# Kernel tuning notes

Hardware: AMD Instinct MI355X
Metric: run time of the kernel (lower is better)

Reference implementation:

```python
import jax, jax.numpy as jnp
import numpy as np

D_MODEL = 1024
D_INNER = 2048   # expand * d_model
D_STATE = 16
D_CONV = 4
DT_RANK = 64     # ceil(d_model / 16)
BATCH = 4
SEQ = 4096


def setup_inputs() -> dict:
    key = jax.random.key(0)
    ks = jax.random.split(key, 8)
    nrm = lambda k, shape, scale: jax.random.normal(k, shape, jnp.float32) * scale
    # dt_proj bias init (inverse softplus of dt in [dt_min, dt_max])
    dt_min, dt_max, dt_floor = 1e-3, 1e-1, 1e-4
    dt = jnp.exp(jax.random.uniform(ks[5], (D_INNER,), jnp.float32)
                 * (np.log(dt_max) - np.log(dt_min)) + np.log(dt_min))
    dt = jnp.clip(dt, dt_floor, None)
    b_dt = dt + jnp.log(-jnp.expm1(-dt))
    # A = diag(1..d_state) per channel, stored as log
    A_log = jnp.broadcast_to(jnp.log(jnp.arange(1, D_STATE + 1, dtype=jnp.float32))[None, :],
                             (D_INNER, D_STATE)).copy()
    dt_std = DT_RANK ** -0.5
    return {
        "x": nrm(ks[0], (BATCH, SEQ, D_MODEL), 1.0),
        "W_in": nrm(ks[1], (2 * D_INNER, D_MODEL), 0.02),
        "conv_w": nrm(ks[2], (D_INNER, 1, D_CONV), 0.2),
        "conv_b": jnp.zeros((D_INNER,), jnp.float32),
        "W_x": nrm(ks[3], (DT_RANK + 2 * D_STATE, D_INNER), 0.02),
        "W_dt": jax.random.uniform(ks[4], (D_INNER, DT_RANK), jnp.float32, -dt_std, dt_std),
        "b_dt": b_dt,
        "A_log": A_log,
        "D": jnp.ones((D_INNER,), jnp.float32),
        "W_out": nrm(ks[6], (D_MODEL, D_INNER), 0.02),
    }


def reference(x, W_in, conv_w, conv_b, W_x, W_dt, b_dt, A_log, D, W_out):
    B, T, _ = x.shape
    silu = jax.nn.silu
    # in_proj -> (x_inner, z)
    xz = jnp.einsum('btd,ed->bte', x, W_in)          # (B,T,2*d_inner)
    x_inner, z = jnp.split(xz, 2, axis=-1)
    # causal depthwise conv1d (pad left d_conv-1, equiv to torch pad+slice[:T])
    xp = jnp.pad(x_inner.transpose(0, 2, 1), ((0, 0), (0, 0), (D_CONV - 1, 0)))
    xc = jax.lax.conv_general_dilated(xp, conv_w, (1,), 'VALID',
                                      feature_group_count=D_INNER)  # (B,d_inner,T)
    x_conv = silu(xc + conv_b[None, :, None]).transpose(0, 2, 1)    # (B,T,d_inner)
    # x_proj -> dt_rank | B | C
    x_dbl = jnp.einsum('btd,ed->bte', x_conv, W_x)
    dt_r, B_ssm, C_ssm = jnp.split(x_dbl, [DT_RANK, DT_RANK + D_STATE], axis=-1)
    dt = jax.nn.softplus(jnp.einsum('btr,dr->btd', dt_r, W_dt) + b_dt)  # (B,T,d_inner)
    A = -jnp.exp(A_log)                                                 # (d_inner,d_state)
    # selective scan over time
    def step(s, inp):
        x_t, dt_t, B_t, C_t = inp              # (B,d_inner),(B,d_inner),(B,d_state),(B,d_state)
        dA = jnp.exp(dt_t[:, :, None] * A[None])              # (B,d_inner,d_state)
        s = s * dA + (dt_t * x_t)[:, :, None] * B_t[:, None, :]
        y_t = jnp.einsum('bds,bs->bd', s, C_t)
        return s, y_t

    s0 = jnp.zeros((B, D_INNER, D_STATE), jnp.float32)
    scan_in = (x_conv.transpose(1, 0, 2), dt.transpose(1, 0, 2),
               B_ssm.transpose(1, 0, 2), C_ssm.transpose(1, 0, 2))
    _, ys = jax.lax.scan(step, s0, scan_in)    # (T,B,d_inner)
    y = ys.transpose(1, 0, 2)
    y = y * silu(z) + D * x_conv
    out = jnp.einsum('btd,ed->bte', y, W_out)  # (B,T,d_model)
    return out
```

## Files before the change

kernel.cpp:

```cpp
#include <hip/hip_runtime.h>
#include <hip/hip_bf16.h>
#include <hip/hip_fp16.h>

#define SEQ    4096
#define DMODEL 1024
#define DINNER 2048
#define DSTATE 16
#define DTRANK 64
#define NC     64
#define CL     64
#define SPLITK 4

typedef __bf16 v8bf  __attribute__((ext_vector_type(8)));
typedef float  f32x4 __attribute__((ext_vector_type(4)));
typedef unsigned short u16x8 __attribute__((ext_vector_type(8)));

static __device__ __forceinline__ float bfu2f(unsigned short u) {
    union { float f; unsigned int i; } c; c.i = ((unsigned int)u) << 16; return c.f;
}
static __device__ __forceinline__ unsigned short f2bfu(float f) {
    union { float f; unsigned int i; } c; c.f = f;
    unsigned int r = c.i + 0x7FFFu + ((c.i >> 16) & 1u);
    return (unsigned short)(r >> 16);
}
static __device__ __forceinline__ float h2f(unsigned short u) {
    __half h; *reinterpret_cast<unsigned short*>(&h) = u; return __half2float(h);
}
static __device__ __forceinline__ unsigned short f2h(float f) {
    __half h = __float2half(f); return *reinterpret_cast<unsigned short*>(&h);
}
static __device__ __forceinline__ float softplus_fast(float v) {
    return fmaxf(v, 0.f) + __logf(1.f + __expf(-fabsf(v)));
}

static __device__ __forceinline__ void gload_lds16(const void* g, void* l) {
    __builtin_amdgcn_global_load_lds(
        (const __attribute__((address_space(1))) unsigned int*)g,
        (__attribute__((address_space(3))) unsigned int*)l, 16, 0, 0);
}

static __device__ __forceinline__ void pow16(float e1, float* pw) {
    const float e2 = e1 * e1, e4 = e2 * e2, e8 = e4 * e4;
    pw[0] = e1;        pw[1] = e2;        pw[2] = e2 * e1;   pw[3] = e4;
    pw[4] = e4 * e1;   pw[5] = e4 * e2;   pw[6] = e4 * pw[2]; pw[7] = e8;
    pw[8] = e8 * e1;   pw[9] = e8 * e2;   pw[10] = e8 * pw[2]; pw[11] = e8 * e4;
    pw[12] = e8 * pw[4]; pw[13] = e8 * pw[5]; pw[14] = e8 * pw[6]; pw[15] = e8 * e8;
}

__global__ void detect_kernel(const void* __restrict__ x, int* __restrict__ flag)
{
    const float f = ((const float*)x)[threadIdx.x];
    const float a = fabsf(f);
    const bool ok = (a < 1e20f) && (a > 1e-20f);
    unsigned long long m = __ballot(ok);
    if (threadIdx.x == 0) *flag = (__popcll(m) >= 48) ? 1 : 0;
}

__global__ void prep_kernel(const unsigned short* __restrict__ a_log_b,
                            int* __restrict__ sflag)
{
    __shared__ int ok_sh;
    if (threadIdx.x == 0) ok_sh = 1;
    __syncthreads();
    int ok = 1;
    for (int i = threadIdx.x; i < DINNER * DSTATE; i += 256) {
        const float A = __expf(bfu2f(a_log_b[i]));
        const float n = (float)((i & 15) + 1);
        if (fabsf(A - n) > 0.02f * n) ok = 0;
    }
    if (!ok) atomicAnd(&ok_sh, 0);
    __syncthreads();
    if (threadIdx.x == 0) *sflag = ok_sh;
}

__global__ __launch_bounds__(256) void cvt_kernel(
    const void* __restrict__ src, size_t src_off,
    unsigned short* __restrict__ dst, int n, const int* __restrict__ flagp)
{
    const int f32 = *flagp;
    const int stride = gridDim.x * 256;
    if (f32) {
        const float* s = (const float*)src + src_off;
        for (int i = blockIdx.x * 256 + threadIdx.x; i < n; i += stride)
            dst[i] = f2bfu(s[i]);
    } else {
        const unsigned short* s = (const unsigned short*)src + src_off;
        for (int i = blockIdx.x * 256 + threadIdx.x; i < n; i += stride)
            dst[i] = s[i];
    }
}

struct CvtBatch {
    const void* src[9];
    unsigned short* dst[9];
    int n[9];
};
__global__ __launch_bounds__(256) void cvt9_kernel(CvtBatch jb,
                                                   const int* __restrict__ flagp)
{
    const int f32 = *flagp;
    const int t = blockIdx.y;
    const int n = jb.n[t];
    unsigned short* __restrict__ dst = jb.dst[t];
    const int stride = gridDim.x * 256;
    if (f32) {
        const float* __restrict__ s = (const float*)jb.src[t];
        for (int i = blockIdx.x * 256 + threadIdx.x; i < n; i += stride)
            dst[i] = f2bfu(s[i]);
    } else {
        const unsigned short* __restrict__ s = (const unsigned short*)jb.src[t];
        for (int i = blockIdx.x * 256 + threadIdx.x; i < n; i += stride)
            dst[i] = s[i];
    }
}

__global__ __launch_bounds__(256) void gemm_db(
    const unsigned short* __restrict__ A, int lda,
    const unsigned short* __restrict__ B, int ldb,
    void* __restrict__ Cbase, int row0c, int ldc, int c_ext,
    int N, int K, const int* __restrict__ flagp, int nfast)
{
    __shared__ __align__(16) unsigned short SM[4 * 128 * 64];

    const int cf32 = c_ext ? *flagp : 0;

    const int tid  = threadIdx.x;
    const int lane = tid & 63;
    const int wave = tid >> 6;
    const int wr   = wave >> 1;
    const int wc   = wave & 1;

    const int bid = blockIdx.y * gridDim.x + blockIdx.x;
    const int r   = bid & 7;
    const int q   = bid >> 3;
    int mt, nt;
    if (nfast) {
        const int npx = gridDim.x;
        const int qm  = q / npx;
        mt = r * (gridDim.y >> 3) + qm;
        nt = q - qm * npx;
    } else {
        const int mpx = gridDim.y >> 3;
        mt = r * mpx + (q & (mpx - 1));
        nt = q / mpx;
    }
    const int m0  = mt * 128;
    const int n0  = nt * 128;

    f32x4 acc[4][4] = {};

    const int r32 = tid >> 3;
    const int c8  = tid & 7;

    const unsigned short* Arow = A + (size_t)m0 * lda;
    const unsigned short* Brow = B + (size_t)n0 * ldb;

#define STAGE_DB(buf, k0)                                                      \
    {                                                                          \
        _Pragma("unroll")                                                      \
        for (int h = 0; h < 4; ++h) {                                          \
            const int rr = r32 + h * 32;                                       \
            const int lg = (c8 ^ (rr & 7)) * 8;                                \
            gload_lds16(&Arow[(size_t)rr * lda + (k0) + lg],                   \
                        &SM[(buf) * 8192 + rr * 64 + c8 * 8]);                 \
            gload_lds16(&Brow[(size_t)rr * ldb + (k0) + lg],                   \
                        &SM[16384 + (buf) * 8192 + rr * 64 + c8 * 8]);         \
        }                                                                      \
    }

    STAGE_DB(0, 0);
    const int NT = K >> 6;
    int cur = 0;

    for (int kt = 0; kt < NT; ++kt) {
        if (kt + 1 < NT) {
            STAGE_DB(cur ^ 1, (kt + 1) * 64);
            asm volatile("s_waitcnt vmcnt(8)" ::: "memory");
        } else {
            asm volatile("s_waitcnt vmcnt(0)" ::: "memory");
        }
        __builtin_amdgcn_s_barrier();

        const unsigned short* Ab = &SM[cur * 8192];
        const unsigned short* Bb = &SM[16384 + cur * 8192];
        const int lm = lane & 15;
        const int g  = lane >> 4;
#pragma unroll
        for (int ks = 0; ks < 2; ++ks) {
            v8bf a_frag[4], b_frag[4];
#pragma unroll
            for (int i = 0; i < 4; ++i) {
                const int ra = wr * 64 + i * 16 + lm;
                const int rb = wc * 64 + i * 16 + lm;
                a_frag[i] = *reinterpret_cast<const v8bf*>(
                    &Ab[ra * 64 + (((ks * 4 + g) ^ (ra & 7))) * 8]);
                b_frag[i] = *reinterpret_cast<const v8bf*>(
                    &Bb[rb * 64 + (((ks * 4 + g) ^ (rb & 7))) * 8]);
            }
#pragma unroll
            for (int i = 0; i < 4; ++i)
#pragma unroll
                for (int j = 0; j < 4; ++j)
                    acc[i][j] = __builtin_amdgcn_mfma_f32_16x16x32_bf16(
                        a_frag[i], b_frag[j], acc[i][j], 0, 0, 0);
        }
        asm volatile("" ::: "memory");
        __builtin_amdgcn_s_barrier();
        cur ^= 1;
    }
#undef STAGE_DB

    float* eb = reinterpret_cast<float*>(SM);
    {
        const int lm = lane & 15;
        const int lr = (lane >> 4) * 4;
#pragma unroll
        for (int i = 0; i < 4; ++i)
#pragma unroll
            for (int j = 0; j < 4; ++j) {
                const int cl = wc * 64 + j * 16 + lm;
#pragma unroll
                for (int q2 = 0; q2 < 4; ++q2) {
                    const int row = wr * 64 + i * 16 + lr + q2;
                    eb[row * 128 + (cl ^ ((row & 7) << 2))] = acc[i][j][q2];
                }
            }
    }
    __syncthreads();
#pragma unroll
    for (int r0 = 0; r0 < 8; ++r0) {
        const int row = (tid >> 4) + r0 * 16;
        const int cb2 = (tid & 15) * 8;
        const int sw  = (row & 7) << 2;
        const f32x4 v0 = *reinterpret_cast<const f32x4*>(&eb[row * 128 + (cb2 ^ sw)]);
        const f32x4 v1 = *reinterpret_cast<const f32x4*>(&eb[row * 128 + ((cb2 + 4) ^ sw)]);
        const size_t gr = (size_t)(row0c + m0 + row) * ldc + n0 + cb2;
        if (cf32) {
            __builtin_nontemporal_store(v0, reinterpret_cast<f32x4*>(&((float*)Cbase)[gr]));
            __builtin_nontemporal_store(v1, reinterpret_cast<f32x4*>(&((float*)Cbase)[gr + 4]));
        } else {
            u16x8 o;
#pragma unroll
            for (int k = 0; k < 4; ++k) { o[k] = f2bfu(v0[k]); o[4 + k] = f2bfu(v1[k]); }
            *reinterpret_cast<u16x8*>(&((unsigned short*)Cbase)[gr]) = o;
        }
    }
}

__global__ __launch_bounds__(256) void gemm_dt(
    const unsigned short* __restrict__ A, int lda,
    const unsigned short* __restrict__ B, int ldb,
    unsigned short* __restrict__ Cbase, int ldc,
    const unsigned short* __restrict__ bias)
{
    __shared__ __align__(16) unsigned short SM[2 * 128 * 64];

    const int tid  = threadIdx.x;
    const int lane = tid & 63;
    const int wave = tid >> 6;
    const int wr   = wave >> 1;
    const int wc   = wave & 1;
    const int m0   = blockIdx.y * 128;
    const int n0   = blockIdx.x * 128;

    f32x4 acc[4][4] = {};

    const int r32 = tid >> 3;
    const int c8  = tid & 7;

    unsigned short* As = SM;
    unsigned short* Bs = SM + 8192;
    {
#pragma unroll
        for (int h = 0; h < 4; ++h) {
            const int rr = r32 + h * 32;
            const int lg = (c8 ^ (rr & 7)) * 8;
            gload_lds16(&A[(size_t)(m0 + rr) * lda + lg], &As[rr * 64 + c8 * 8]);
            gload_lds16(&B[(size_t)(n0 + rr) * ldb + lg], &Bs[rr * 64 + c8 * 8]);
        }
        __syncthreads();

        const int lm = lane & 15;
        const int g  = lane >> 4;
#pragma unroll
        for (int ks = 0; ks < 2; ++ks) {
            v8bf a_frag[4], b_frag[4];
#pragma unroll
            for (int i = 0; i < 4; ++i) {
                const int ra = wr * 64 + i * 16 + lm;
                const int rb = wc * 64 + i * 16 + lm;
                a_frag[i] = *reinterpret_cast<const v8bf*>(
                    &As[ra * 64 + (((ks * 4 + g) ^ (ra & 7))) * 8]);
                b_frag[i] = *reinterpret_cast<const v8bf*>(
                    &Bs[rb * 64 + (((ks * 4 + g) ^ (rb & 7))) * 8]);
            }
#pragma unroll
            for (int i = 0; i < 4; ++i)
#pragma unroll
                for (int j = 0; j < 4; ++j)
                    acc[i][j] = __builtin_amdgcn_mfma_f32_16x16x32_bf16(
                        a_frag[i], b_frag[j], acc[i][j], 0, 0, 0);
        }
    }

    __syncthreads();
    unsigned short* eb16 = SM;
    {
        const int lm = lane & 15;
        const int lr = (lane >> 4) * 4;
#pragma unroll
        for (int i = 0; i < 4; ++i)
#pragma unroll
            for (int j = 0; j < 4; ++j) {
                const int cl = wc * 64 + j * 16 + lm;
                const float bv = bfu2f(bias[n0 + cl]);
#pragma unroll
                for (int q = 0; q < 4; ++q) {
                    const int row = wr * 64 + i * 16 + lr + q;
                    const int pos = row * 128 +
                        ((((cl >> 3) ^ (row & 7)) << 3) | (cl & 7));
                    eb16[pos] = f2h(softplus_fast(acc[i][j][q] + bv));
                }
            }
    }
    __syncthreads();
#pragma unroll
    for (int r0 = 0; r0 < 8; ++r0) {
        const int row = (tid >> 4) + r0 * 16;
        const int ch  = tid & 15;
        const u16x8 v = *reinterpret_cast<const u16x8*>(
            &eb16[row * 128 + ((ch ^ (row & 7)) << 3)]);
        *reinterpret_cast<u16x8*>(
            &Cbase[(size_t)(m0 + row) * ldc + n0 + ch * 8]) = v;
    }
}

__global__ __launch_bounds__(256) void gemm_splitk(
    const unsigned short* __restrict__ A, int lda,
    const unsigned short* __restrict__ B, int ldb,
    float* __restrict__ part, int Mrows,
    int N, int kchunk)
{
    __shared__ __align__(16) unsigned short SM[4 * 128 * 64];

    const int tid  = threadIdx.x;
    const int lane = tid & 63;
    const int wave = tid >> 6;
    const int wr   = wave >> 1;
    const int wc   = wave & 1;
    const int m0   = blockIdx.y * 128;
    const int split = blockIdx.z;
    const int kbeg = split * kchunk;

    f32x4 acc[4][4] = {};

    const int r32 = tid >> 3;
    const int c8  = tid & 7;

#define STAGE_SK(buf, k0)                                                      \
    {                                                                          \
        _Pragma("unroll")                                                      \
        for (int h = 0; h < 4; ++h) {                                          \
            const int rr = r32 + h * 32;                                       \
            const int lg = (c8 ^ (rr & 7)) * 8;                                \
            gload_lds16(&A[(size_t)(m0 + rr) * lda + (k0) + lg],               \
                        &SM[(buf) * 8192 + rr * 64 + c8 * 8]);                 \
            gload_lds16(&B[(size_t)rr * ldb + (k0) + lg],                      \
                        &SM[16384 + (buf) * 8192 + rr * 64 + c8 * 8]);         \
        }                                                                      \
    }

    STAGE_SK(0, kbeg);
    const int NT = kchunk >> 6;
    int cur = 0;

    for (int kt = 0; kt < NT; ++kt) {
        if (kt + 1 < NT) {
            STAGE_SK(cur ^ 1, kbeg + (kt + 1) * 64);
            asm volatile("s_waitcnt vmcnt(8)" ::: "memory");
        } else {
            asm volatile("s_waitcnt vmcnt(0)" ::: "memory");
        }
        __builtin_amdgcn_s_barrier();

        const unsigned short* Ab = &SM[cur * 8192];
        const unsigned short* Bb = &SM[16384 + cur * 8192];
        const int lm = lane & 15;
        const int g  = lane >> 4;
#pragma unroll
        for (int ks = 0; ks < 2; ++ks) {
            v8bf a_frag[4], b_frag[4];
#pragma unroll
            for (int i = 0; i < 4; ++i) {
                const int ra = wr * 64 + i * 16 + lm;
                const int rb = wc * 64 + i * 16 + lm;
                a_frag[i] = *reinterpret_cast<const v8bf*>(
                    &Ab[ra * 64 + (((ks * 4 + g) ^ (ra & 7))) * 8]);
                b_frag[i] = *reinterpret_cast<const v8bf*>(
                    &Bb[rb * 64 + (((ks * 4 + g) ^ (rb & 7))) * 8]);
            }
#pragma unroll
            for (int i = 0; i < 4; ++i)
#pragma unroll
                for (int j = 0; j < 4; ++j)
                    acc[i][j] = __builtin_amdgcn_mfma_f32_16x16x32_bf16(
                        a_frag[i], b_frag[j], acc[i][j], 0, 0, 0);
        }
        asm volatile("" ::: "memory");
        __builtin_amdgcn_s_barrier();
        cur ^= 1;
    }
#undef STAGE_SK

    const int lm = lane & 15;
    const int lr = (lane >> 4) * 4;
    float* dst = part + (size_t)split * Mrows * 96;
#pragma unroll
    for (int i = 0; i < 4; ++i) {
#pragma unroll
        for (int j = 0; j < 4; ++j) {
            const int col = wc * 64 + j * 16 + lm;
            if (col >= N) continue;
#pragma unroll
            for (int q = 0; q < 4; ++q) {
                const int row = m0 + wr * 64 + i * 16 + lr + q;
                dst[(size_t)row * 96 + col] = acc[i][j][q];
            }
        }
    }
}

__global__ __launch_bounds__(256) void splitk_reduce(
    const float* __restrict__ part, unsigned short* __restrict__ dst,
    float* __restrict__ bcf, int n)
{
    const int i = blockIdx.x * 256 + threadIdx.x;
    if (i >= n) return;
    float s = 0.f;
#pragma unroll
    for (int k = 0; k < SPLITK; ++k) s += part[(size_t)k * n + i];
    dst[i] = f2bfu(s);
    const int m = i / 96;
    const int col = i - m * 96;
    if (col >= 64) bcf[(size_t)m * 32 + (col - 64)] = s;
}

__global__ __launch_bounds__(256) void conv_silu_kernel(
    const unsigned short* __restrict__ xz,
    const unsigned short* __restrict__ cw,
    const unsigned short* __restrict__ cb,
    unsigned short* __restrict__ xc)
{
    const int idx = blockIdx.x * 256 + threadIdx.x;
    const int d4 = idx & 511;
    const int m = idx >> 9;
    const int t = m & (SEQ - 1);
    const int d = d4 * 4;

    const u16x8 w0 = *reinterpret_cast<const u16x8*>(&cw[d * 4]);
    const u16x8 w1 = *reinterpret_cast<const u16x8*>(&cw[d * 4 + 8]);
    const uint2 bb = *reinterpret_cast<const uint2*>(&cb[d]);
    float s0 = bfu2f((unsigned short)(bb.x & 0xffff));
    float s1 = bfu2f((unsigned short)(bb.x >> 16));
    float s2 = bfu2f((unsigned short)(bb.y & 0xffff));
    float s3 = bfu2f((unsigned short)(bb.y >> 16));
#pragma unroll
    for (int j = 0; j < 4; ++j) {
        const int tt = t - 3 + j;
        if (tt >= 0) {
            const uint2 xv = *reinterpret_cast<const uint2*>(
                &xz[(size_t)(m - 3 + j) * 4096 + d]);
            s0 += bfu2f(w0[j])     * bfu2f((unsigned short)(xv.x & 0xffff));
            s1 += bfu2f(w0[4 + j]) * bfu2f((unsigned short)(xv.x >> 16));
            s2 += bfu2f(w1[j])     * bfu2f((unsigned short)(xv.y & 0xffff));
            s3 += bfu2f(w1[4 + j]) * bfu2f((unsigned short)(xv.y >> 16));
        }
    }
    const float g0 = s0 / (1.f + __expf(-s0));
    const float g1 = s1 / (1.f + __expf(-s1));
    const float g2 = s2 / (1.f + __expf(-s2));
    const float g3 = s3 / (1.f + __expf(-s3));
    uint2 o;
    o.x = (unsigned int)f2bfu(g0) | ((unsigned int)f2bfu(g1) << 16);
    o.y = (unsigned int)f2bfu(g2) | ((unsigned int)f2bfu(g3) << 16);
    *reinterpret_cast<uint2*>(&xc[(size_t)m * 2048 + d]) = o;
}

__global__ __launch_bounds__(256) void scan_local_kernel(
    const unsigned short* __restrict__ xz,
    const unsigned short* __restrict__ xconv,
    const float* __restrict__ bcf,
    const unsigned short* __restrict__ A_log,
    unsigned short* __restrict__ S,
    float* __restrict__ sumdt,
    const int* __restrict__ sflagp)
{
    __shared__ __align__(16) float bs[CL * 16];

    const int gid = blockIdx.x * 256 + threadIdx.x;
    const int d = gid & (DINNER - 1);
    const int c = (gid >> 11) & (NC - 1);
    const int b = gid >> 17;
    const int fast = *sflagp;
    const size_t mb = (size_t)b * SEQ + c * CL;

    {
        const int t4 = threadIdx.x >> 2;
        const int q4 = threadIdx.x & 3;
        *reinterpret_cast<f32x4*>(&bs[t4 * 16 + q4 * 4]) =
            *reinterpret_cast<const f32x4*>(&bcf[(mb + t4) * 32 + q4 * 4]);
    }
    __syncthreads();

    float st[16];
#pragma unroll
    for (int s = 0; s < 16; ++s) st[s] = 0.f;
    float sd = 0.f;

    float Ar[16];
    if (!fast) {
#pragma unroll
        for (int s = 0; s < 16; ++s) Ar[s] = -__expf(bfu2f(A_log[d * DSTATE + s]));
    }

    const unsigned short* dtp = xz + mb * 4096 + d;
    const unsigned short* xp  = xconv + mb * DINNER + d;
    unsigned short dt_c = *dtp;
    unsigned short x_c  = *xp;

#pragma unroll 2
    for (int t = 0; t < CL; ++t) {
        const unsigned short dt_n = dtp[(size_t)(t + 1) * 4096];
        const unsigned short x_n  = xp[(size_t)(t + 1) * DINNER];
        const float dt = h2f(dt_c);
        const float x  = bfu2f(x_c);
        const f32x4 B0 = *reinterpret_cast<const f32x4*>(&bs[t * 16]);
        const f32x4 B1 = *reinterpret_cast<const f32x4*>(&bs[t * 16 + 4]);
        const f32x4 B2 = *reinterpret_cast<const f32x4*>(&bs[t * 16 + 8]);
        const f32x4 B3 = *reinterpret_cast<const f32x4*>(&bs[t * 16 + 12]);
        const float du = dt * x;
        float pw[16];
        if (fast) {
            pow16(__expf(-dt), pw);
        } else {
#pragma unroll
            for (int s = 0; s < 16; ++s) pw[s] = __expf(dt * Ar[s]);
        }
#pragma unroll
        for (int s = 0; s < 4; ++s) st[s]      = st[s]      * pw[s]      + du * B0[s];
#pragma unroll
        for (int s = 0; s < 4; ++s) st[4 + s]  = st[4 + s]  * pw[4 + s]  + du * B1[s];
#pragma unroll
        for (int s = 0; s < 4; ++s) st[8 + s]  = st[8 + s]  * pw[8 + s]  + du * B2[s];
#pragma unroll
        for (int s = 0; s < 4; ++s) st[12 + s] = st[12 + s] * pw[12 + s] + du * B3[s];
        sd += dt;
        dt_c = dt_n; x_c = x_n;
    }
    const size_t o = (((size_t)b * NC + c) * DINNER + d) * DSTATE;
    u16x8 h0, h1;
#pragma unroll
    for (int s = 0; s < 8; ++s) { h0[s] = f2h(st[s]); h1[s] = f2h(st[8 + s]); }
    *reinterpret_cast<u16x8*>(&S[o]) = h0;
    *reinterpret_cast<u16x8*>(&S[o + 8]) = h1;
    sumdt[((size_t)b * NC + c) * DINNER + d] = sd;
}

__global__ __launch_bounds__(256) void scan_carry_kernel(
    const unsigned short* __restrict__ A_log,
    unsigned short* __restrict__ S,
    const float* __restrict__ sumdt)
{
    const int gid = blockIdx.x * 256 + threadIdx.x;
    const int s = gid & 15;
    const int d = (gid >> 4) & (DINNER - 1);
    const int b = gid >> 15;

    const float A = -__expf(bfu2f(A_log[d * DSTATE + s]));
    float carry = 0.f;
    for (int c = 0; c < NC; ++c) {
        const size_t o = (((size_t)b * NC + c) * DINNER + d) * DSTATE + s;
        const float se = h2f(S[o]);
        S[o] = f2h(carry);
        carry = carry * __expf(A * sumdt[((size_t)b * NC + c) * DINNER + d]) + se;
    }
}

__global__ __launch_bounds__(256) void scan_final_kernel(
    unsigned short* __restrict__ xz,
    const unsigned short* __restrict__ xconv,
    const float* __restrict__ bcf,
    const unsigned short* __restrict__ A_log,
    const unsigned short* __restrict__ Dvec,
    const unsigned short* __restrict__ S,
    const int* __restrict__ sflagp)
{
    __shared__ __align__(16) float bs[CL * 32];

    const int gid = blockIdx.x * 256 + threadIdx.x;
    const int d = gid & (DINNER - 1);
    const int c = (gid >> 11) & (NC - 1);
    const int b = gid >> 17;
    const int fast = *sflagp;
    const size_t mb = (size_t)b * SEQ + c * CL;

    {
        const int i8 = threadIdx.x * 8;
        *reinterpret_cast<f32x4*>(&bs[i8]) =
            *reinterpret_cast<const f32x4*>(&bcf[mb * 32 + i8]);
        *reinterpret_cast<f32x4*>(&bs[i8 + 4]) =
            *reinterpret_cast<const f32x4*>(&bcf[mb * 32 + i8 + 4]);
    }
    __syncthreads();

    const float Dv = bfu2f(Dvec[d]);
    float st[16];
    const size_t o = (((size_t)b * NC + c) * DINNER + d) * DSTATE;
    {
        const u16x8 h0 = *reinterpret_cast<const u16x8*>(&S[o]);
        const u16x8 h1 = *reinterpret_cast<const u16x8*>(&S[o + 8]);
#pragma unroll
        for (int s = 0; s < 8; ++s) { st[s] = h2f(h0[s]); st[8 + s] = h2f(h1[s]); }
    }

    float Ar[16];
    if (!fast) {
#pragma unroll
        for (int s = 0; s < 16; ++s) Ar[s] = -__expf(bfu2f(A_log[d * DSTATE + s]));
    }

    unsigned short* dtp = xz + mb * 4096 + d;
    const unsigned short* xp = xconv + mb * DINNER + d;
    const unsigned short* zp = xz + mb * 4096 + DINNER + d;
    unsigned short dt_c = *dtp;
    unsigned short x_c  = *xp;
    unsigned short z_c  = *zp;

#pragma unroll 2
    for (int t = 0; t < CL; ++t) {
        const unsigned short dt_n = dtp[(size_t)(t + 1) * 4096];
        const unsigned short x_n  = xp[(size_t)(t + 1) * DINNER];
        const unsigned short z_n  = zp[(size_t)(t + 1) * 4096];
        const float dt = h2f(dt_c);
        const float x  = bfu2f(x_c);
        const f32x4 B0 = *reinterpret_cast<const f32x4*>(&bs[t * 32]);
        const f32x4 B1 = *reinterpret_cast<const f32x4*>(&bs[t * 32 + 4]);
        const f32x4 B2 = *reinterpret_cast<const f32x4*>(&bs[t * 32 + 8]);
        const f32x4 B3 = *reinterpret_cast<const f32x4*>(&bs[t * 32 + 12]);
        const f32x4 C0 = *reinterpret_cast<const f32x4*>(&bs[t * 32 + 16]);
        const f32x4 C1 = *reinterpret_cast<const f32x4*>(&bs[t * 32 + 20]);
        const f32x4 C2 = *reinterpret_cast<const f32x4*>(&bs[t * 32 + 24]);
        const f32x4 C3 = *reinterpret_cast<const f32x4*>(&bs[t * 32 + 28]);
        const float du = dt * x;
        float pw[16];
        if (fast) {
            pow16(__expf(-dt), pw);
        } else {
#pragma unroll
            for (int s = 0; s < 16; ++s) pw[s] = __expf(dt * Ar[s]);
        }
        float p0 = 0.f, p1 = 0.f, p2 = 0.f, p3 = 0.f;
#pragma unroll
        for (int s = 0; s < 4; ++s) {
            st[s] = st[s] * pw[s] + du * B0[s];           p0 += st[s] * C0[s];
        }
#pragma unroll
        for (int s = 0; s < 4; ++s) {
            st[4 + s] = st[4 + s] * pw[4 + s] + du * B1[s];   p1 += st[4 + s] * C1[s];
        }
#pragma unroll
        for (int s = 0; s < 4; ++s) {
            st[8 + s] = st[8 + s] * pw[8 + s] + du * B2[s];   p2 += st[8 + s] * C2[s];
        }
#pragma unroll
        for (int s = 0; s < 4; ++s) {
            st[12 + s] = st[12 + s] * pw[12 + s] + du * B3[s]; p3 += st[12 + s] * C3[s];
        }
        const float p = (p0 + p1) + (p2 + p3);
        const float z = bfu2f(z_c);
        const float sig = 1.f / (1.f + __expf(-z));
        dtp[(size_t)t * 4096] = f2bfu(p * (z * sig) + Dv * x);
        dt_c = dt_n; x_c = x_n; z_c = z_n;
    }
}

extern "C" void kernel_launch(void* const* d_in, const int* in_sizes, int n_in,
                              void* d_out, int out_size, void* d_ws, size_t ws_size,
                              hipStream_t stream)
{
    const void* x     = d_in[0];
    const void* W_in  = d_in[1];
    const void* convw = d_in[2];
    const void* convb = d_in[3];
    const void* W_x   = d_in[4];
    const void* W_dt  = d_in[5];
    const void* b_dt  = d_in[6];
    const void* A_log = d_in[7];
    const void* Dv    = d_in[8];
    const void* W_out = d_in[9];

    char* ws = (char*)d_ws;
    size_t off = 256;
    int* flag  = (int*)ws;
    int* sflag = (int*)ws + 16;
    auto arena = [&](size_t bytes) {
        char* p = ws + off;
        off += (bytes + 255) & ~(size_t)255;
        return p;
    };
    unsigned short* w_in_b  = (unsigned short*)arena((size_t)4096 * 1024 * 2);
    unsigned short* convw_b = (unsigned short*)arena(8192 * 2);
    unsigned short* convb_b = (unsigned short*)arena(2048 * 2);
    unsigned short* w_x_b   = (unsigned short*)arena((size_t)96 * 2048 * 2);
    unsigned short* w_dt_b  = (unsigned short*)arena((size_t)2048 * 64 * 2);
    unsigned short* b_dt_b  = (unsigned short*)arena(2048 * 2);
    unsigned short* a_log_b = (unsigned short*)arena((size_t)2048 * 16 * 2);
    unsigned short* dv_b    = (unsigned short*)arena(2048 * 2);
    unsigned short* w_out_b = (unsigned short*)arena((size_t)1024 * 2048 * 2);
    const size_t fixed = off;

    const size_t U_per_b  = (size_t)SEQ * 1024 * 2;
    const size_t per_batch =
        (size_t)SEQ * 4096 * 2 + (size_t)SEQ * 2048 * 2 + (size_t)SEQ * 96 * 2 +
        U_per_b;
    int CB = 4;
    while (CB > 1 && fixed + (size_t)CB * per_batch > ws_size) CB >>= 1;
    const int nchunks = 4 / CB;
    const int Mc = CB * SEQ;

    unsigned short* xz    = (unsigned short*)(ws + fixed);
    unsigned short* xconv = xz + (size_t)Mc * 4096;
    unsigned short* xdbl  = xconv + (size_t)Mc * 2048;
    char*           U     = (char*)(xdbl + (size_t)Mc * 96);
    unsigned short* x_bf  = (unsigned short*)U;
    float*          xpart = (float*)U;
    float*          bcf   = (float*)(U + (size_t)SPLITK * Mc * 96 * 4);
    unsigned short* S     = (unsigned short*)U;
    float*          sumdt = (float*)(U + (size_t)CB * NC * 2048 * DSTATE * 2);

    detect_kernel<<<1, 64, 0, stream>>>(x, flag);

    CvtBatch jb;
    jb.src[0] = W_in;  jb.dst[0] = w_in_b;  jb.n[0] = 4096 * 1024;
    jb.src[1] = convw; jb.dst[1] = convw_b; jb.n[1] = 8192;
    jb.src[2] = convb; jb.dst[2] = convb_b; jb.n[2] = 2048;
    jb.src[3] = W_x;   jb.dst[3] = w_x_b;   jb.n[3] = 96 * 2048;
    jb.src[4] = W_dt;  jb.dst[4] = w_dt_b;  jb.n[4] = 2048 * 64;
    jb.src[5] = b_dt;  jb.dst[5] = b_dt_b;  jb.n[5] = 2048;
    jb.src[6] = A_log; jb.dst[6] = a_log_b; jb.n[6] = 2048 * 16;
    jb.src[7] = Dv;    jb.dst[7] = dv_b;    jb.n[7] = 2048;
    jb.src[8] = W_out; jb.dst[8] = w_out_b; jb.n[8] = 1024 * 2048;
    cvt9_kernel<<<dim3(256, 9), 256, 0, stream>>>(jb, flag);
    prep_kernel<<<1, 256, 0, stream>>>(a_log_b, sflag);

    for (int cchunk = 0; cchunk < nchunks; ++cchunk) {
        const int row0 = cchunk * Mc;

        cvt_kernel<<<4096, 256, 0, stream>>>(
            x, (size_t)row0 * DMODEL, x_bf, Mc * DMODEL, flag);

        gemm_db<<<dim3(4096 / 128, Mc / 128), 256, 0, stream>>>(
            x_bf, DMODEL, w_in_b, DMODEL, xz, 0, 4096, 0, 4096, DMODEL, flag, 0);

        conv_silu_kernel<<<(Mc * DINNER) / 1024, 256, 0, stream>>>(
            xz, convw_b, convb_b, xconv);

        gemm_splitk<<<dim3(1, Mc / 128, SPLITK), 256, 0, stream>>>(
            xconv, DINNER, w_x_b, DINNER, xpart, Mc, 96, DINNER / SPLITK);
        splitk_reduce<<<(Mc * 96 + 255) / 256, 256, 0, stream>>>(
            xpart, xdbl, bcf, Mc * 96);

        gemm_dt<<<dim3(DINNER / 128, Mc / 128), 256, 0, stream>>>(
            xdbl, 96, w_dt_b, DTRANK, xz, 4096, b_dt_b);

        scan_local_kernel<<<(CB * NC * DINNER) / 256, 256, 0, stream>>>(
            xz, xconv, bcf, a_log_b, S, sumdt, sflag);
        scan_carry_kernel<<<(CB * DINNER * DSTATE) / 256, 256, 0, stream>>>(
            a_log_b, S, sumdt);
        scan_final_kernel<<<(CB * NC * DINNER) / 256, 256, 0, stream>>>(
            xz, xconv, bcf, a_log_b, dv_b, S, sflag);

        gemm_db<<<dim3(DMODEL / 128, Mc / 128), 256, 0, stream>>>(
            xz, 4096, w_out_b, DINNER, d_out, row0, DMODEL, 1,
            DMODEL, DINNER, flag, 1);
    }
}
```

Before: 582.2 us.

## Compute intra-chunk scan output in first pass, apply carry correction afterward

The first scan pass now produces the zero-initial-state output y (including the D skip term) and writes the running cumulative dt into the xconv buffer as fp16. The final pass is replaced by a lighter fix pass that adds C·(carry·exp(A·cumdt)) gated by silu(z), so it no longer recomputes the full state recurrence. This removes one sequential 16-state recurrence but adds extra fp16 round-trips of the partial output and cumulative dt, which may cost accuracy.

```diff
diff --git a/kernel.cpp b/kernel.cpp
--- a/kernel.cpp
+++ b/kernel.cpp
@@ -487,15 +487,16 @@
 }
 
 __global__ __launch_bounds__(256) void scan_local_kernel(
-    const unsigned short* __restrict__ xz,
-    const unsigned short* __restrict__ xconv,
+    unsigned short* __restrict__ xz,
+    unsigned short* __restrict__ xconv,
     const float* __restrict__ bcf,
     const unsigned short* __restrict__ A_log,
     unsigned short* __restrict__ S,
     float* __restrict__ sumdt,
+    const unsigned short* __restrict__ Dvec,
     const int* __restrict__ sflagp)
 {
-    __shared__ __align__(16) float bs[CL * 16];
+    __shared__ __align__(16) float bs[CL * 32];
 
     const int gid = blockIdx.x * 256 + threadIdx.x;
     const int d = gid & (DINNER - 1);
@@ -505,106 +506,6 @@
     const size_t mb = (size_t)b * SEQ + c * CL;
 
     {
-        const int t4 = threadIdx.x >> 2;
-        const int q4 = threadIdx.x & 3;
-        *reinterpret_cast<f32x4*>(&bs[t4 * 16 + q4 * 4]) =
-            *reinterpret_cast<const f32x4*>(&bcf[(mb + t4) * 32 + q4 * 4]);
-    }
-    __syncthreads();
-
-    float st[16];
-#pragma unroll
-    for (int s = 0; s < 16; ++s) st[s] = 0.f;
-    float sd = 0.f;
-
-    float Ar[16];
-    if (!fast) {
-#pragma unroll
-        for (int s = 0; s < 16; ++s) Ar[s] = -__expf(bfu2f(A_log[d * DSTATE + s]));
-    }
-
-    const unsigned short* dtp = xz + mb * 4096 + d;
-    const unsigned short* xp  = xconv + mb * DINNER + d;
-    unsigned short dt_c = *dtp;
-    unsigned short x_c  = *xp;
-
-#pragma unroll 2
-    for (int t = 0; t < CL; ++t) {
-        const unsigned short dt_n = dtp[(size_t)(t + 1) * 4096];
-        const unsigned short x_n  = xp[(size_t)(t + 1) * DINNER];
-        const float dt = h2f(dt_c);
-        const float x  = bfu2f(x_c);
-        const f32x4 B0 = *reinterpret_cast<const f32x4*>(&bs[t * 16]);
-        const f32x4 B1 = *reinterpret_cast<const f32x4*>(&bs[t * 16 + 4]);
-        const f32x4 B2 = *reinterpret_cast<const f32x4*>(&bs[t * 16 + 8]);
-        const f32x4 B3 = *reinterpret_cast<const f32x4*>(&bs[t * 16 + 12]);
-        const float du = dt * x;
-        float pw[16];
-        if (fast) {
-            pow16(__expf(-dt), pw);
-        } else {
-#pragma unroll
-            for (int s = 0; s < 16; ++s) pw[s] = __expf(dt * Ar[s]);
-        }
-#pragma unroll
-        for (int s = 0; s < 4; ++s) st[s]      = st[s]      * pw[s]      + du * B0[s];
-#pragma unroll
-        for (int s = 0; s < 4; ++s) st[4 + s]  = st[4 + s]  * pw[4 + s]  + du * B1[s];
-#pragma unroll
-        for (int s = 0; s < 4; ++s) st[8 + s]  = st[8 + s]  * pw[8 + s]  + du * B2[s];
-#pragma unroll
-        for (int s = 0; s < 4; ++s) st[12 + s] = st[12 + s] * pw[12 + s] + du * B3[s];
-        sd += dt;
-        dt_c = dt_n; x_c = x_n;
-    }
-    const size_t o = (((size_t)b * NC + c) * DINNER + d) * DSTATE;
-    u16x8 h0, h1;
-#pragma unroll
-    for (int s = 0; s < 8; ++s) { h0[s] = f2h(st[s]); h1[s] = f2h(st[8 + s]); }
-    *reinterpret_cast<u16x8*>(&S[o]) = h0;
-    *reinterpret_cast<u16x8*>(&S[o + 8]) = h1;
-    sumdt[((size_t)b * NC + c) * DINNER + d] = sd;
-}
-
-__global__ __launch_bounds__(256) void scan_carry_kernel(
-    const unsigned short* __restrict__ A_log,
-    unsigned short* __restrict__ S,
-    const float* __restrict__ sumdt)
-{
-    const int gid = blockIdx.x * 256 + threadIdx.x;
-    const int s = gid & 15;
-    const int d = (gid >> 4) & (DINNER - 1);
-    const int b = gid >> 15;
-
-    const float A = -__expf(bfu2f(A_log[d * DSTATE + s]));
-    float carry = 0.f;
-    for (int c = 0; c < NC; ++c) {
-        const size_t o = (((size_t)b * NC + c) * DINNER + d) * DSTATE + s;
-        const float se = h2f(S[o]);
-        S[o] = f2h(carry);
-        carry = carry * __expf(A * sumdt[((size_t)b * NC + c) * DINNER + d]) + se;
-    }
-}
-
-__global__ __launch_bounds__(256) void scan_final_kernel(
-    unsigned short* __restrict__ xz,
-    const unsigned short* __restrict__ xconv,
-    const float* __restrict__ bcf,
-    const unsigned short* __restrict__ A_log,
-    const unsigned short* __restrict__ Dvec,
-    const unsigned short* __restrict__ S,
-    const int* __restrict__ sflagp)
-{
-    __shared__ __align__(16) float bs[CL * 32];
-
-    const int gid = blockIdx.x * 256 + threadIdx.x;
-    const int d = gid & (DINNER - 1);
-    const int c = (gid >> 11) & (NC - 1);
-    const int b = gid >> 17;
-    const int fast = *sflagp;
-    const size_t mb = (size_t)b * SEQ + c * CL;
-
-    {
         const int i8 = threadIdx.x * 8;
         *reinterpret_cast<f32x4*>(&bs[i8]) =
             *reinterpret_cast<const f32x4*>(&bcf[mb * 32 + i8]);
@@ -615,13 +516,9 @@
 
     const float Dv = bfu2f(Dvec[d]);
     float st[16];
-    const size_t o = (((size_t)b * NC + c) * DINNER + d) * DSTATE;
-    {
-        const u16x8 h0 = *reinterpret_cast<const u16x8*>(&S[o]);
-        const u16x8 h1 = *reinterpret_cast<const u16x8*>(&S[o + 8]);
-#pragma unroll
-        for (int s = 0; s < 8; ++s) { st[s] = h2f(h0[s]); st[8 + s] = h2f(h1[s]); }
-    }
+#pragma unroll
+    for (int s = 0; s < 16; ++s) st[s] = 0.f;
+    float sd = 0.f;
 
     float Ar[16];
     if (!fast) {
@@ -630,7 +527,7 @@
     }
 
     unsigned short* dtp = xz + mb * 4096 + d;
-    const unsigned short* xp = xconv + mb * DINNER + d;
+    unsigned short* xp  = xconv + mb * DINNER + d;
     const unsigned short* zp = xz + mb * 4096 + DINNER + d;
     unsigned short dt_c = *dtp;
     unsigned short x_c  = *xp;
@@ -677,10 +574,120 @@
             st[12 + s] = st[12 + s] * pw[12 + s] + du * B3[s]; p3 += st[12 + s] * C3[s];
         }
         const float p = (p0 + p1) + (p2 + p3);
+        sd += dt;
         const float z = bfu2f(z_c);
         const float sig = 1.f / (1.f + __expf(-z));
-        dtp[(size_t)t * 4096] = f2bfu(p * (z * sig) + Dv * x);
+        dtp[(size_t)t * 4096] = f2h(p * (z * sig) + Dv * x);
+        xp[(size_t)t * DINNER] = f2h(sd);
         dt_c = dt_n; x_c = x_n; z_c = z_n;
+    }
+    const size_t o = (((size_t)b * NC + c) * DINNER + d) * DSTATE;
+    u16x8 h0, h1;
+#pragma unroll
+    for (int s = 0; s < 8; ++s) { h0[s] = f2h(st[s]); h1[s] = f2h(st[8 + s]); }
+    *reinterpret_cast<u16x8*>(&S[o]) = h0;
+    *reinterpret_cast<u16x8*>(&S[o + 8]) = h1;
+    sumdt[((size_t)b * NC + c) * DINNER + d] = sd;
+}
+
+__global__ __launch_bounds__(256) void scan_carry_kernel(
+    const unsigned short* __restrict__ A_log,
+    unsigned short* __restrict__ S,
+    const float* __restrict__ sumdt)
+{
+    const int gid = blockIdx.x * 256 + threadIdx.x;
+    const int s = gid & 15;
+    const int d = (gid >> 4) & (DINNER - 1);
+    const int b = gid >> 15;
+
+    const float A = -__expf(bfu2f(A_log[d * DSTATE + s]));
+    float carry = 0.f;
+    for (int c = 0; c < NC; ++c) {
+        const size_t o = (((size_t)b * NC + c) * DINNER + d) * DSTATE + s;
+        const float se = h2f(S[o]);
+        S[o] = f2h(carry);
+        carry = carry * __expf(A * sumdt[((size_t)b * NC + c) * DINNER + d]) + se;
+    }
+}
+
+__global__ __launch_bounds__(256) void scan_fix_kernel(
+    unsigned short* __restrict__ xz,
+    const unsigned short* __restrict__ xconv,
+    const float* __restrict__ bcf,
+    const unsigned short* __restrict__ A_log,
+    const unsigned short* __restrict__ S,
+    const int* __restrict__ sflagp)
+{
+    __shared__ __align__(16) float cs[CL * 16];
+
+    const int gid = blockIdx.x * 256 + threadIdx.x;
+    const int d = gid & (DINNER - 1);
+    const int c = (gid >> 11) & (NC - 1);
+    const int b = gid >> 17;
+    const int fast = *sflagp;
+    const size_t mb = (size_t)b * SEQ + c * CL;
+
+    {
+        const int t4 = threadIdx.x >> 2;
+        const int q4 = threadIdx.x & 3;
+        *reinterpret_cast<f32x4*>(&cs[t4 * 16 + q4 * 4]) =
+            *reinterpret_cast<const f32x4*>(&bcf[(mb + t4) * 32 + 16 + q4 * 4]);
+    }
+    __syncthreads();
+
+    float q[16];
+    const size_t o = (((size_t)b * NC + c) * DINNER + d) * DSTATE;
+    {
+        const u16x8 h0 = *reinterpret_cast<const u16x8*>(&S[o]);
+        const u16x8 h1 = *reinterpret_cast<const u16x8*>(&S[o + 8]);
+#pragma unroll
+        for (int s = 0; s < 8; ++s) { q[s] = h2f(h0[s]); q[8 + s] = h2f(h1[s]); }
+    }
+
+    float Ar[16];
+    if (!fast) {
+#pragma unroll
+        for (int s = 0; s < 16; ++s) Ar[s] = -__expf(bfu2f(A_log[d * DSTATE + s]));
+    }
+
+    unsigned short* ypp = xz + mb * 4096 + d;
+    const unsigned short* cdp = xconv + mb * DINNER + d;
+    const unsigned short* zp  = xz + mb * 4096 + DINNER + d;
+    unsigned short yp_c = *ypp;
+    unsigned short cd_c = *cdp;
+    unsigned short z_c  = *zp;
+
+#pragma unroll 2
+    for (int t = 0; t < CL; ++t) {
+        const unsigned short yp_n = ypp[(size_t)(t + 1) * 4096];
+        const unsigned short cd_n = cdp[(size_t)(t + 1) * DINNER];
+        const unsigned short z_n  = zp[(size_t)(t + 1) * 4096];
+        const float cd = h2f(cd_c);
+        const f32x4 C0 = *reinterpret_cast<const f32x4*>(&cs[t * 16]);
+        const f32x4 C1 = *reinterpret_cast<const f32x4*>(&cs[t * 16 + 4]);
+        const f32x4 C2 = *reinterpret_cast<const f32x4*>(&cs[t * 16 + 8]);
+        const f32x4 C3 = *reinterpret_cast<const f32x4*>(&cs[t * 16 + 12]);
+        float pw[16];
+        if (fast) {
+            pow16(__expf(-cd), pw);
+        } else {
+#pragma unroll
+            for (int s = 0; s < 16; ++s) pw[s] = __expf(cd * Ar[s]);
+        }
+        float p0 = 0.f, p1 = 0.f, p2 = 0.f, p3 = 0.f;
+#pragma unroll
+        for (int s = 0; s < 4; ++s) p0 += q[s]      * pw[s]      * C0[s];
+#pragma unroll
+        for (int s = 0; s < 4; ++s) p1 += q[4 + s]  * pw[4 + s]  * C1[s];
+#pragma unroll
+        for (int s = 0; s < 4; ++s) p2 += q[8 + s]  * pw[8 + s]  * C2[s];
+#pragma unroll
+        for (int s = 0; s < 4; ++s) p3 += q[12 + s] * pw[12 + s] * C3[s];
+        const float corr = (p0 + p1) + (p2 + p3);
+        const float z = bfu2f(z_c);
+        const float sig = 1.f / (1.f + __expf(-z));
+        ypp[(size_t)t * 4096] = f2bfu(h2f(yp_c) + corr * (z * sig));
+        yp_c = yp_n; cd_c = cd_n; z_c = z_n;
     }
 }
 
@@ -774,11 +781,11 @@
             xdbl, 96, w_dt_b, DTRANK, xz, 4096, b_dt_b);
 
         scan_local_kernel<<<(CB * NC * DINNER) / 256, 256, 0, stream>>>(
-            xz, xconv, bcf, a_log_b, S, sumdt, sflag);
+            xz, xconv, bcf, a_log_b, S, sumdt, dv_b, sflag);
         scan_carry_kernel<<<(CB * DINNER * DSTATE) / 256, 256, 0, stream>>>(
             a_log_b, S, sumdt);
-        scan_final_kernel<<<(CB * NC * DINNER) / 256, 256, 0, stream>>>(
-            xz, xconv, bcf, a_log_b, dv_b, S, sflag);
+        scan_fix_kernel<<<(CB * NC * DINNER) / 256, 256, 0, stream>>>(
+            xz, xconv, bcf, a_log_b, S, sflag);
 
         gemm_db<<<dim3(DMODEL / 128, Mc / 128), 256, 0, stream>>>(
             xz, 4096, w_out_b, DINNER, d_out, row0, DMODEL, 1,
```

Measured after the change: 585.5 us. About the same (+0.6%).

## Add 256x128-tile 512-thread GEMM kernel for output projection

Applied to the files above, without the earlier changes.

Replaces the generic 128x128 double-buffered GEMM used for the output projection with a dedicated kernel that uses 8 waves and a 256-row M tile, sharing each B tile across twice as many rows. The epilogue is split into two halves so it fits in the shared buffer. This is meant to cut B-operand reloads and raise MFMA work per block for the K=2048 output GEMM. In exchange it uses more LDS per block and launches fewer blocks, which may lower occupancy and leave fewer blocks to spread across CUs. The nfast branch is removed from gemm_db because only the input projection still uses it.

```diff
diff --git a/kernel.cpp b/kernel.cpp
--- a/kernel.cpp
+++ b/kernel.cpp
@@ -118,7 +118,7 @@
     const unsigned short* __restrict__ A, int lda,
     const unsigned short* __restrict__ B, int ldb,
     void* __restrict__ Cbase, int row0c, int ldc, int c_ext,
-    int N, int K, const int* __restrict__ flagp, int nfast)
+    int N, int K, const int* __restrict__ flagp)
 {
     __shared__ __align__(16) unsigned short SM[4 * 128 * 64];
 
@@ -133,17 +133,9 @@
     const int bid = blockIdx.y * gridDim.x + blockIdx.x;
     const int r   = bid & 7;
     const int q   = bid >> 3;
-    int mt, nt;
-    if (nfast) {
-        const int npx = gridDim.x;
-        const int qm  = q / npx;
-        mt = r * (gridDim.y >> 3) + qm;
-        nt = q - qm * npx;
-    } else {
-        const int mpx = gridDim.y >> 3;
-        mt = r * mpx + (q & (mpx - 1));
-        nt = q / mpx;
-    }
+    const int mpx = gridDim.y >> 3;
+    const int mt  = r * mpx + (q & (mpx - 1));
+    const int nt  = q / mpx;
     const int m0  = mt * 128;
     const int n0  = nt * 128;
 
@@ -243,6 +235,141 @@
 #pragma unroll
             for (int k = 0; k < 4; ++k) { o[k] = f2bfu(v0[k]); o[4 + k] = f2bfu(v1[k]); }
             *reinterpret_cast<u16x8*>(&((unsigned short*)Cbase)[gr]) = o;
+        }
+    }
+}
+
+__global__ __launch_bounds__(512) void gemm_out(
+    const unsigned short* __restrict__ A, int lda,
+    const unsigned short* __restrict__ B, int ldb,
+    void* __restrict__ Cbase, int row0c, int ldc, int c_ext,
+    int K, const int* __restrict__ flagp)
+{
+    __shared__ __align__(16) unsigned short SM[2 * 384 * 64];
+
+    const int cf32 = c_ext ? *flagp : 0;
+
+    const int tid  = threadIdx.x;
+    const int lane = tid & 63;
+    const int wave = tid >> 6;
+    const int wr   = wave >> 1;
+    const int wc   = wave & 1;
+
+    const int bid = blockIdx.y * gridDim.x + blockIdx.x;
+    const int r   = bid & 7;
+    const int q   = bid >> 3;
+    const int npx = gridDim.x;
+    const int qm  = q / npx;
+    const int nt  = q - qm * npx;
+    const int mt  = r * (gridDim.y >> 3) + qm;
+    const int m0  = mt * 256;
+    const int n0  = nt * 128;
+
+    f32x4 acc[4][4] = {};
+
+    const int r64 = tid >> 3;
+    const int c8  = tid & 7;
+
+    const unsigned short* Arow = A + (size_t)m0 * lda;
+    const unsigned short* Brow = B + (size_t)n0 * ldb;
+
+#define STAGE_O(buf, k0)                                                       \
+    {                                                                          \
+        _Pragma("unroll")                                                      \
+        for (int h = 0; h < 4; ++h) {                                          \
+            const int rr = r64 + h * 64;                                       \
+            const int lg = (c8 ^ (rr & 7)) * 8;                                \
+            gload_lds16(&Arow[(size_t)rr * lda + (k0) + lg],                   \
+                        &SM[(buf) * 16384 + rr * 64 + c8 * 8]);                \
+        }                                                                      \
+        _Pragma("unroll")                                                      \
+        for (int h = 0; h < 2; ++h) {                                          \
+            const int rr = r64 + h * 64;                                       \
+            const int lg = (c8 ^ (rr & 7)) * 8;                                \
+            gload_lds16(&Brow[(size_t)rr * ldb + (k0) + lg],                   \
+                        &SM[32768 + (buf) * 8192 + rr * 64 + c8 * 8]);         \
+        }                                                                      \
+    }
+
+    STAGE_O(0, 0);
+    const int NT = K >> 6;
+    int cur = 0;
+
+    for (int kt = 0; kt < NT; ++kt) {
+        if (kt + 1 < NT) {
+            STAGE_O(cur ^ 1, (kt + 1) * 64);
+            asm volatile("s_waitcnt vmcnt(6)" ::: "memory");
+        } else {
+            asm volatile("s_waitcnt vmcnt(0)" ::: "memory");
+        }
+        __builtin_amdgcn_s_barrier();
+
+        const unsigned short* Ab = &SM[cur * 16384];
+        const unsigned short* Bb = &SM[32768 + cur * 8192];
+        const int lm = lane & 15;
+        const int g  = lane >> 4;
+#pragma unroll
+        for (int ks = 0; ks < 2; ++ks) {
+            v8bf a_frag[4], b_frag[4];
+#pragma unroll
+            for (int i = 0; i < 4; ++i) {
+                const int ra = wr * 64 + i * 16 + lm;
+                const int rb = wc * 64 + i * 16 + lm;
+                a_frag[i] = *reinterpret_cast<const v8bf*>(
+                    &Ab[ra * 64 + (((ks * 4 + g) ^ (ra & 7))) * 8]);
+                b_frag[i] = *reinterpret_cast<const v8bf*>(
+                    &Bb[rb * 64 + (((ks * 4 + g) ^ (rb & 7))) * 8]);
+            }
+#pragma unroll
+            for (int i = 0; i < 4; ++i)
+#pragma unroll
+                for (int j = 0; j < 4; ++j)
+                    acc[i][j] = __builtin_amdgcn_mfma_f32_16x16x32_bf16(
+                        a_frag[i], b_frag[j], acc[i][j], 0, 0, 0);
+        }
+        asm volatile("" ::: "memory");
+        __builtin_amdgcn_s_barrier();
+        cur ^= 1;
+    }
+#undef STAGE_O
+
+    float* eb = reinterpret_cast<float*>(SM);
+    const int lm = lane & 15;
+    const int lr = (lane >> 4) * 4;
+#pragma unroll
+    for (int h = 0; h < 2; ++h) {
+        __syncthreads();
+        if ((wr >> 1) == h) {
+#pragma unroll
+            for (int i = 0; i < 4; ++i)
+#pragma unroll
+                for (int j = 0; j < 4; ++j) {
+                    const int cl = wc * 64 + j * 16 + lm;
+#pragma unroll
+                    for (int q2 = 0; q2 < 4; ++q2) {
+                        const int row = (wr & 1) * 64 + i * 16 + lr + q2;
+                        eb[row * 128 + (cl ^ ((row & 7) << 2))] = acc[i][j][q2];
+                    }
+                }
+        }
+        __syncthreads();
+#pragma unroll
+        for (int r0 = 0; r0 < 4; ++r0) {
+            const int row = (tid >> 4) + r0 * 32;
+            const int cb2 = (tid & 15) * 8;
+            const int sw  = (row & 7) << 2;
+            const f32x4 v0 = *reinterpret_cast<const f32x4*>(&eb[row * 128 + (cb2 ^ sw)]);
+            const f32x4 v1 = *reinterpret_cast<const f32x4*>(&eb[row * 128 + ((cb2 + 4) ^ sw)]);
+            const size_t gr = (size_t)(row0c + m0 + h * 128 + row) * ldc + n0 + cb2;
+            if (cf32) {
+                __builtin_nontemporal_store(v0, reinterpret_cast<f32x4*>(&((float*)Cbase)[gr]));
+                __builtin_nontemporal_store(v1, reinterpret_cast<f32x4*>(&((float*)Cbase)[gr + 4]));
+            } else {
+                u16x8 o;
+#pragma unroll
+                for (int k = 0; k < 4; ++k) { o[k] = f2bfu(v0[k]); o[4 + k] = f2bfu(v1[k]); }
+                *reinterpret_cast<u16x8*>(&((unsigned short*)Cbase)[gr]) = o;
+            }
         }
     }
 }
@@ -760,7 +887,7 @@
             x, (size_t)row0 * DMODEL, x_bf, Mc * DMODEL, flag);
 
         gemm_db<<<dim3(4096 / 128, Mc / 128), 256, 0, stream>>>(
-            x_bf, DMODEL, w_in_b, DMODEL, xz, 0, 4096, 0, 4096, DMODEL, flag, 0);
+            x_bf, DMODEL, w_in_b, DMODEL, xz, 0, 4096, 0, 4096, DMODEL, flag);
 
         conv_silu_kernel<<<(Mc * DINNER) / 1024, 256, 0, stream>>>(
             xz, convw_b, convb_b, xconv);
@@ -780,8 +907,7 @@
         scan_final_kernel<<<(CB * NC * DINNER) / 256, 256, 0, stream>>>(
             xz, xconv, bcf, a_log_b, dv_b, S, sflag);
 
-        gemm_db<<<dim3(DMODEL / 128, Mc / 128), 256, 0, stream>>>(
-            xz, 4096, w_out_b, DINNER, d_out, row0, DMODEL, 1,
-            DMODEL, DINNER, flag, 1);
-    }
-}
+        gemm_out<<<dim3(DMODEL / 128, Mc / 256), 512, 0, stream>>>(
+            xz, 4096, w_out_b, DINNER, d_out, row0, DMODEL, 1, DINNER, flag);
+    }
+}
```

Result: slower. 600.5 us (+3.1%).
